# Optimization experiments

Hardware: AMD Instinct MI355X
Metric: run time of the kernel (lower is better)

## Reference

```python
import jax, jax.numpy as jnp
import numpy as np

B, N, C, H, NRES = 32, 1024, 384, 1024, 20
NTAB = 21  # 20 aa + unknown, per AlphaFold residue_constants


def setup_inputs() -> dict:
    key = jax.random.key(0)
    ks = jax.random.split(key, 16)
    s = 0.02
    inp = {}
    inp['act'] = jax.random.normal(ks[0], (B, N, C), jnp.float32)
    inp['angles'] = jax.random.normal(ks[1], (B, N, 7, 2), jnp.float32)
    inp['rigids'] = jax.random.normal(ks[2], (B, N, 7), jnp.float32)
    inp['fixed_mask'] = jax.random.randint(ks[3], (B, N), 0, 2, jnp.int32)
    inp['seq_t'] = jax.random.randint(ks[4], (B, N), 0, NRES, jnp.int32)
    inp['residx_atom37_to_atom14'] = jax.random.randint(ks[5], (B, N, 37), 0, 14, jnp.int32)
    inp['ln_g'] = jnp.ones((C,), jnp.float32)
    inp['ln_b'] = jnp.zeros((C,), jnp.float32)
    inp['w1'] = jax.random.normal(ks[6], (C, H), jnp.float32) * s
    inp['b1'] = jnp.zeros((H,), jnp.float32)
    inp['w2'] = jax.random.normal(ks[7], (H, H), jnp.float32) * s
    inp['b2'] = jnp.zeros((H,), jnp.float32)
    inp['w3'] = jax.random.normal(ks[8], (H, NRES), jnp.float32) * s
    inp['b3'] = jnp.zeros((NRES,), jnp.float32)
    # stand-in residue_constants tables (same shapes/dtypes as AlphaFold's)
    inp['default_frames'] = jax.random.normal(ks[9], (NTAB, 8, 4, 4), jnp.float32)
    inp['group_idx'] = jax.random.randint(ks[10], (NTAB, 14), 0, 8, jnp.int32)
    inp['atom14_mask'] = (jax.random.uniform(ks[11], (NTAB, 14)) > 0.3).astype(jnp.float32)
    inp['atom37_mask'] = (jax.random.uniform(ks[12], (NTAB, 37)) > 0.3).astype(jnp.float32)
    inp['lit_positions'] = jax.random.normal(ks[13], (NTAB, 14, 3), jnp.float32)
    return inp


def quat_to_rot(q):
    q = q / jnp.sqrt(jnp.sum(q * q, axis=-1, keepdims=True) + 1e-8)
    w, x, y, z = q[..., 0], q[..., 1], q[..., 2], q[..., 3]
    r = jnp.stack([
        1 - 2 * (y * y + z * z), 2 * (x * y - w * z), 2 * (x * z + w * y),
        2 * (x * y + w * z), 1 - 2 * (x * x + z * z), 2 * (y * z - w * x),
        2 * (x * z - w * y), 2 * (y * z + w * x), 1 - 2 * (x * x + y * y)
    ], axis=-1)
    return r.reshape(q.shape[:-1] + (3, 3))


def compose(r1, t1, r2, t2):
    # rigid composition: (r1, t1) o (r2, t2)
    return (jnp.einsum('...ij,...jk->...ik', r1, r2),
            jnp.einsum('...ij,...j->...i', r1, t2) + t1)


def reference(act, angles, rigids, fixed_mask, seq_t, residx_atom37_to_atom14,
              ln_g, ln_b, w1, b1, w2, b2, w3, b3,
              default_frames, group_idx, atom14_mask, atom37_mask, lit_positions):
    # --- small MLP head ---
    mu = jnp.mean(act, axis=-1, keepdims=True)
    var = jnp.var(act, axis=-1, keepdims=True)
    h = (act - mu) / jnp.sqrt(var + 1e-5) * ln_g + ln_b
    h = jax.nn.relu(h @ w1 + b1)
    h = jax.nn.relu(h @ w2 + b2)
    logits = h @ w3 + b3                                # [B,N,20]
    p_0t = jax.nn.softmax(logits, axis=-1)
    seq0 = jnp.argmax(p_0t, axis=-1).astype(jnp.int32)
    seq0 = seq0 * (1 - fixed_mask) + seq_t * fixed_mask  # [B,N]

    # --- backbone frame from quaternion rigids ---
    rb = quat_to_rot(rigids[..., :4])                    # [B,N,3,3]
    tb = rigids[..., 4:]                                 # [B,N,3]

    # --- torsion_angles_to_frames ---
    df = default_frames[seq0]                            # [B,N,8,4,4]
    dr, dt = df[..., :3, :3], df[..., :3, 3]
    sin, cos = angles[..., 0], angles[..., 1]            # [B,N,7]
    z1 = jnp.zeros_like(sin[..., :1])
    sin8 = jnp.concatenate([z1, sin], axis=-1)           # backbone group has angle 0
    cos8 = jnp.concatenate([jnp.ones_like(z1), cos], axis=-1)
    zz, oo = jnp.zeros_like(sin8), jnp.ones_like(sin8)
    rx = jnp.stack([oo, zz, zz, zz, cos8, -sin8, zz, sin8, cos8], axis=-1)
    rx = rx.reshape(sin8.shape + (3, 3))                 # rotation about x-axis
    fr = jnp.einsum('bngij,bngjk->bngik', dr, rx)        # frames to backbone (pre-chain)
    ft = dt
    # chain chi2->chi1, chi3->chi2, chi4->chi3
    r5, t5 = compose(fr[..., 4, :, :], ft[..., 4, :], fr[..., 5, :, :], ft[..., 5, :])
    r6, t6 = compose(r5, t5, fr[..., 6, :, :], ft[..., 6, :])
    r7, t7 = compose(r6, t6, fr[..., 7, :, :], ft[..., 7, :])
    frot = jnp.concatenate([fr[..., :5, :, :], r5[..., None, :, :], r6[..., None, :, :], r7[..., None, :, :]], axis=-3)
    ftr = jnp.concatenate([ft[..., :5, :], t5[..., None, :], t6[..., None, :], t7[..., None, :]], axis=-2)
    grot, gtr = compose(rb[..., None, :, :], tb[..., None, :], frot, ftr)  # [B,N,8,3,3],[B,N,8,3]

    # --- frames_and_literature_positions_to_atom14_pos ---
    gi = group_idx[seq0]                                 # [B,N,14]
    ar = jnp.take_along_axis(grot, jnp.broadcast_to(gi[..., None, None], gi.shape + (3, 3)), axis=2)
    at = jnp.take_along_axis(gtr, jnp.broadcast_to(gi[..., None], gi.shape + (3,)), axis=2)
    lit = lit_positions[seq0]                            # [B,N,14,3]
    m14 = atom14_mask[seq0]                              # [B,N,14]
    pred = (jnp.einsum('bnaij,bnaj->bnai', ar, lit) + at) * m14[..., None]

    # --- atom14 -> atom37 gather ---
    idx = residx_atom37_to_atom14
    final = jnp.take_along_axis(pred, jnp.broadcast_to(idx[..., None], idx.shape + (3,)), axis=2)
    m37 = atom37_mask[seq0]                              # [B,N,37]
    return logits, seq0, pred, final, m14, m37
```

## Files before the change

kernel.cpp:

```cpp
#include <hip/hip_runtime.h>
#include <math.h>

#define B_ 32
#define N_ 1024
#define C_ 384
#define H_ 1024
#define NRES 20
#define NTAB 21
#define M_TOTAL (B_*N_)
#define BK 32

typedef __attribute__((ext_vector_type(8))) short bf16x8;
typedef __attribute__((ext_vector_type(4))) float f32x4;

#define GLOAD_LDS(gptr, lptr) \
    __builtin_amdgcn_global_load_lds( \
        (const __attribute__((address_space(1))) void*)(gptr), \
        (__attribute__((address_space(3))) void*)(lptr), 16, 0, 0)

__device__ inline short bf16_rne(float v) {
    unsigned u = __float_as_uint(v);
    unsigned r = u + 0x7fffu + ((u >> 16) & 1u);
    return (short)(r >> 16);
}
__device__ inline void split2(float v, short& h, short& l) {
    unsigned u = __float_as_uint(v);
    unsigned r = (u + 0x7fffu + ((u >> 16) & 1u)) & 0xffff0000u;
    h = (short)(r >> 16);
    l = bf16_rne(v - __uint_as_float(r));
}

__global__ __launch_bounds__(256) void ln_split_kernel(const float* __restrict__ act,
                                                       const float* __restrict__ lng,
                                                       const float* __restrict__ lnb,
                                                       short* __restrict__ Xh,
                                                       short* __restrict__ Xl) {
    int wave = threadIdx.x >> 6;
    int lane = threadIdx.x & 63;
    int row  = blockIdx.x * 4 + wave;
    const float* x = act + (size_t)row * C_;
    float v[6];
    float s = 0.f;
#pragma unroll
    for (int i = 0; i < 6; i++) { v[i] = x[lane + i*64]; s += v[i]; }
#pragma unroll
    for (int off = 32; off > 0; off >>= 1) s += __shfl_xor(s, off, 64);
    float mu = s * (1.0f/384.0f);
    float vs = 0.f;
#pragma unroll
    for (int i = 0; i < 6; i++) { float d = v[i]-mu; vs += d*d; }
#pragma unroll
    for (int off = 32; off > 0; off >>= 1) vs += __shfl_xor(vs, off, 64);
    float rstd = 1.0f / sqrtf(vs * (1.0f/384.0f) + 1e-5f);
#pragma unroll
    for (int i = 0; i < 6; i++) {
        int col = lane + i*64;
        float y = (v[i] - mu) * rstd * lng[col] + lnb[col];
        short h, l; split2(y, h, l);
        Xh[(size_t)row * C_ + col] = h;
        Xl[(size_t)row * C_ + col] = l;
    }
}

__global__ __launch_bounds__(256) void conv_w_kernel(const float* __restrict__ w,
                                                     short* __restrict__ th,
                                                     short* __restrict__ tl,
                                                     int K, int N, int Npad) {
    __shared__ float t[32][33];
    int n0 = blockIdx.x * 32, k0 = blockIdx.y * 32;
    int tx = threadIdx.x & 31, ty = threadIdx.x >> 5;
#pragma unroll
    for (int i = ty; i < 32; i += 8) {
        int k = k0 + i, n = n0 + tx;
        t[i][tx] = (n < N) ? w[(size_t)k * N + n] : 0.f;
    }
    __syncthreads();
#pragma unroll
    for (int i = ty; i < 32; i += 8) {
        int n = n0 + i, k = k0 + tx;
        short h, l; split2(t[tx][i], h, l);
        th[(size_t)n * K + k] = h;
        tl[(size_t)n * K + k] = l;
    }
}

template<bool FUSE>
__global__ __launch_bounds__(512, 2) void presplit_gemm256(
    const short* __restrict__ Ahg, const short* __restrict__ Alg,
    const short* __restrict__ BTh, const short* __restrict__ BTl,
    const float* __restrict__ bias,
    short* __restrict__ Ch, short* __restrict__ Cl,
    int K, int ldc,
    const short* __restrict__ W3h, const short* __restrict__ W3l,
    float* __restrict__ logit_acc, int m0c)
{
    __shared__ short P[4][2][256][32];
    const int BUFS = 256*32;
    int tid = threadIdx.x;
    int m0 = blockIdx.x * 256;
    int n0 = blockIdx.y * 256;
    int lane = tid & 63, wv = tid >> 6;
    int wr = wv >> 2, wc = wv & 3;
    int fm = lane & 15, kg = lane >> 4;

    int pl = wv >> 1, hf = wv & 1;
    const short* gsrc = (pl == 0) ? Ahg : (pl == 1) ? Alg : (pl == 2) ? BTh : BTl;
    int base = (pl < 2) ? m0 : n0;
    int swcb = (lane & 3) ^ ((lane >> 3) & 3);
    const short* gp = gsrc + (size_t)(base + hf*128 + (lane >> 2)) * K + swcb * 8;
    short* lpl = &P[pl][0][0][0] + hf * (128*32);

    int sz = (kg ^ ((fm >> 1) & 3)) * 8;
    const short* raH = &P[0][0][wr*128 + fm][0] + sz;
    const short* raL = &P[1][0][wr*128 + fm][0] + sz;
    const short* rbH = &P[2][0][wc*64  + fm][0] + sz;
    const short* rbL = &P[3][0][wc*64  + fm][0] + sz;

#define STAGE(c, bsel, koff) \
    GLOAD_LDS(gp + (size_t)((c)*16) * K + (koff), lpl + (bsel)*BUFS + (c)*512)

#define TRIPLE(ai, aj, AH, AL, BH, BL) { \
    f32x4 cc = acc[ai][aj]; \
    cc = __builtin_amdgcn_mfma_f32_16x16x32_bf16(AL, BH, cc, 0, 0, 0); \
    cc = __builtin_amdgcn_mfma_f32_16x16x32_bf16(AH, BL, cc, 0, 0, 0); \
    cc = __builtin_amdgcn_mfma_f32_16x16x32_bf16(AH, BH, cc, 0, 0, 0); \
    acc[ai][aj] = cc; }

    f32x4 acc[8][4] = {};
    const int NT = K / BK;

#pragma unroll
    for (int c = 0; c < 8; c++) STAGE(c, 0, 0);

    for (int t = 0; t < NT; ++t) {
        int cur = t & 1, nxt = cur ^ 1;
        size_t koff = (size_t)(t + 1) * BK;
        bool pf = (t + 1 < NT);

        bf16x8 a_h[4], a_l[4], b_h[4], b_l[4];

        if (pf) {
            STAGE(0, nxt, koff); STAGE(1, nxt, koff);
            asm volatile("s_waitcnt vmcnt(2)" ::: "memory");
        } else {
            asm volatile("s_waitcnt vmcnt(0)" ::: "memory");
        }
        __builtin_amdgcn_s_barrier();
        __builtin_amdgcn_sched_barrier(0);
#pragma unroll
        for (int i = 0; i < 4; i++) {
            a_h[i] = *(const bf16x8*)(raH + cur*BUFS + i*512);
            a_l[i] = *(const bf16x8*)(raL + cur*BUFS + i*512);
        }
#pragma unroll
        for (int j = 0; j < 2; j++) {
            b_h[j] = *(const bf16x8*)(rbH + cur*BUFS + j*512);
            b_l[j] = *(const bf16x8*)(rbL + cur*BUFS + j*512);
        }
        __builtin_amdgcn_s_setprio(1);
#pragma unroll
        for (int i = 0; i < 4; i++)
#pragma unroll
            for (int j = 0; j < 2; j++) TRIPLE(i, j, a_h[i], a_l[i], b_h[j], b_l[j]);
        __builtin_amdgcn_s_setprio(0);
        __builtin_amdgcn_s_barrier();

        if (pf) { STAGE(2, nxt, koff); STAGE(3, nxt, koff); }
#pragma unroll
        for (int j = 0; j < 2; j++) {
            b_h[2+j] = *(const bf16x8*)(rbH + cur*BUFS + (2+j)*512);
            b_l[2+j] = *(const bf16x8*)(rbL + cur*BUFS + (2+j)*512);
        }
        __builtin_amdgcn_s_barrier();
        __builtin_amdgcn_s_setprio(1);
#pragma unroll
        for (int i = 0; i < 4; i++)
#pragma unroll
            for (int j = 0; j < 2; j++) TRIPLE(i, 2+j, a_h[i], a_l[i], b_h[2+j], b_l[2+j]);
        __builtin_amdgcn_s_setprio(0);
        __builtin_amdgcn_s_barrier();

        if (pf) { STAGE(4, nxt, koff); STAGE(5, nxt, koff); }
#pragma unroll
        for (int i = 0; i < 4; i++) {
            a_h[i] = *(const bf16x8*)(raH + cur*BUFS + (4+i)*512);
            a_l[i] = *(const bf16x8*)(raL + cur*BUFS + (4+i)*512);
        }
        __builtin_amdgcn_s_barrier();
        __builtin_amdgcn_s_setprio(1);
#pragma unroll
        for (int i = 0; i < 4; i++)
#pragma unroll
            for (int j = 0; j < 2; j++) TRIPLE(4+i, j, a_h[i], a_l[i], b_h[j], b_l[j]);
        __builtin_amdgcn_s_setprio(0);
        __builtin_amdgcn_s_barrier();

        if (pf) { STAGE(6, nxt, koff); STAGE(7, nxt, koff); }
        __builtin_amdgcn_s_barrier();
        __builtin_amdgcn_s_setprio(1);
#pragma unroll
        for (int i = 0; i < 4; i++)
#pragma unroll
            for (int j = 0; j < 2; j++) TRIPLE(4+i, 2+j, a_h[i], a_l[i], b_h[2+j], b_l[2+j]);
        __builtin_amdgcn_s_setprio(0);
        __builtin_amdgcn_s_barrier();
    }

    if (!FUSE) {
#pragma unroll
        for (int i = 0; i < 8; i++)
#pragma unroll
            for (int j = 0; j < 4; j++) {
                int col = n0 + wc*64 + j*16 + fm;
                float bs = bias[col];
#pragma unroll
                for (int r2 = 0; r2 < 4; r2++) {
                    int row = m0 + wr*128 + i*16 + kg*4 + r2;
                    float v = fmaxf(acc[i][j][r2] + bs, 0.f);
                    short h, l; split2(v, h, l);
                    Ch[(size_t)row * ldc + col] = h;
                    Cl[(size_t)row * ldc + col] = l;
                }
            }
    } else {
        unsigned* L32 = (unsigned*)&P[0][0][0][0];
#pragma unroll
        for (int h = 0; h < 2; h++) {
            if (wr == h) {
#pragma unroll
                for (int i = 0; i < 8; i++)
#pragma unroll
                    for (int j = 0; j < 4; j++) {
                        int col = wc*64 + j*16 + fm;
                        float bs = bias[n0 + col];
#pragma unroll
                        for (int r2 = 0; r2 < 4; r2++) {
                            int lr = i*16 + kg*4 + r2;
                            float v = fmaxf(acc[i][j][r2] + bs, 0.f);
                            short sh, sl; split2(v, sh, sl);
                            L32[lr*256 + (col ^ ((lr & 15) << 1))] =
                                ((unsigned)(unsigned short)sh << 16) | (unsigned short)sl;
                        }
                    }
            }
            __syncthreads();
            f32x4 pl0 = {}, pl1 = {};
            int rbase = (wv*16 + fm) * 256;
            int swr = fm << 1;
#pragma unroll
            for (int s = 0; s < 8; s++) {
                int kb = s*32 + kg*8;
                bf16x8 A_h, A_l;
#pragma unroll
                for (int c = 0; c < 8; c++) {
                    unsigned u = L32[rbase + ((kb + c) ^ swr)];
                    A_h[c] = (short)(u >> 16);
                    A_l[c] = (short)(u & 0xffffu);
                }
                size_t wk = (size_t)(n0 + kb);
                bf16x8 B0h = *(const bf16x8*)&W3h[(size_t)fm * H_ + wk];
                bf16x8 B0l = *(const bf16x8*)&W3l[(size_t)fm * H_ + wk];
                bf16x8 B1h = *(const bf16x8*)&W3h[(size_t)(16 + fm) * H_ + wk];
                bf16x8 B1l = *(const bf16x8*)&W3l[(size_t)(16 + fm) * H_ + wk];
                pl0 = __builtin_amdgcn_mfma_f32_16x16x32_bf16(A_l, B0h, pl0, 0, 0, 0);
                pl0 = __builtin_amdgcn_mfma_f32_16x16x32_bf16(A_h, B0l, pl0, 0, 0, 0);
                pl0 = __builtin_amdgcn_mfma_f32_16x16x32_bf16(A_h, B0h, pl0, 0, 0, 0);
                pl1 = __builtin_amdgcn_mfma_f32_16x16x32_bf16(A_l, B1h, pl1, 0, 0, 0);
                pl1 = __builtin_amdgcn_mfma_f32_16x16x32_bf16(A_h, B1l, pl1, 0, 0, 0);
                pl1 = __builtin_amdgcn_mfma_f32_16x16x32_bf16(A_h, B1h, pl1, 0, 0, 0);
            }
            int growb = m0c + m0 + h*128 + wv*16 + kg*4;
#pragma unroll
            for (int r2 = 0; r2 < 4; r2++)
                atomicAdd(&logit_acc[(size_t)(growb + r2) * NRES + fm], pl0[r2]);
            if (fm < 4) {
#pragma unroll
                for (int r2 = 0; r2 < 4; r2++)
                    atomicAdd(&logit_acc[(size_t)(growb + r2) * NRES + 16 + fm], pl1[r2]);
            }
            __syncthreads();
        }
    }
#undef STAGE
#undef TRIPLE
}

__global__ __launch_bounds__(256) void argmax_kernel(
    float* __restrict__ logits, const float* __restrict__ b3,
    const int* __restrict__ fixed_mask, const int* __restrict__ seq_t,
    float* __restrict__ seq_out, int* __restrict__ seq_int, int m0c)
{
    int grow = m0c + blockIdx.x * 256 + threadIdx.x;
    float* lg = logits + (size_t)grow * NRES;
    float best = -1e30f; int bi = 0;
#pragma unroll
    for (int n = 0; n < NRES; n++) {
        float s = lg[n] + b3[n];
        lg[n] = s;
        if (s > best) { best = s; bi = n; }
    }
    int fmk = fixed_mask[grow];
    int sv = fmk ? seq_t[grow] : bi;
    seq_int[grow] = sv;
    seq_out[grow] = (float)sv;
}

__global__ __launch_bounds__(256) void geom_atom_kernel(
    const float* __restrict__ angles, const float* __restrict__ rigids,
    const int* __restrict__ seq0i,
    const float* __restrict__ dframes, const int* __restrict__ gidx,
    const float* __restrict__ a14m, const float* __restrict__ litp,
    float* __restrict__ out_pred, float* __restrict__ out_m14)
{
    __shared__ float sdf[NTAB*8*16];
    __shared__ int   sgi[NTAB*14];
    __shared__ float sm14[NTAB*14];
    __shared__ float slit[NTAB*14*3];
    for (int i = threadIdx.x; i < NTAB*128; i += 256) sdf[i] = dframes[i];
    for (int i = threadIdx.x; i < NTAB*14; i += 256) { sgi[i] = gidx[i]; sm14[i] = a14m[i]; }
    for (int i = threadIdx.x; i < NTAB*42; i += 256) slit[i] = litp[i];
    __syncthreads();

    int idx = blockIdx.x * 256 + threadIdx.x;
    int p = idx / 14, a = idx - p * 14;
    int s = seq0i[p];

    const float* rg = rigids + (size_t)p * 7;
    float qw = rg[0], qx = rg[1], qy = rg[2], qz = rg[3];
    float tbx = rg[4], tby = rg[5], tbz = rg[6];
    float qn = 1.0f / sqrtf(qw*qw + qx*qx + qy*qy + qz*qz + 1e-8f);
    qw *= qn; qx *= qn; qy *= qn; qz *= qn;
    float rb[9];
    rb[0] = 1.f - 2.f*(qy*qy + qz*qz); rb[1] = 2.f*(qx*qy - qw*qz); rb[2] = 2.f*(qx*qz + qw*qy);
    rb[3] = 2.f*(qx*qy + qw*qz); rb[4] = 1.f - 2.f*(qx*qx + qz*qz); rb[5] = 2.f*(qy*qz - qw*qx);
    rb[6] = 2.f*(qx*qz - qw*qy); rb[7] = 2.f*(qy*qz + qw*qx); rb[8] = 1.f - 2.f*(qx*qx + qy*qy);

    const float* ang = angles + (size_t)p * 14;
    int g = sgi[s*14 + a];

    auto build = [&](int gg, float* r, float* t) {
        const float* df = &sdf[(s*8 + gg)*16];
        float c, sn;
        if (gg == 0) { c = 1.f; sn = 0.f; }
        else { sn = ang[(gg-1)*2 + 0]; c = ang[(gg-1)*2 + 1]; }
#pragma unroll
        for (int i = 0; i < 3; i++) {
            float d0 = df[i*4+0], d1 = df[i*4+1], d2 = df[i*4+2];
            r[i*3+0] = d0;
            r[i*3+1] = d1*c + d2*sn;
            r[i*3+2] = d2*c - d1*sn;
            t[i] = df[i*4+3];
        }
    };

    float R[9], T[3];
    if (g < 5) {
        build(g, R, T);
    } else {
        build(4, R, T);
        for (int gg = 5; gg <= g; gg++) {
            float f[9], tt[3], r2[9], t2[3];
            build(gg, f, tt);
#pragma unroll
            for (int i = 0; i < 3; i++) {
#pragma unroll
                for (int j = 0; j < 3; j++)
                    r2[i*3+j] = R[i*3+0]*f[0*3+j] + R[i*3+1]*f[1*3+j] + R[i*3+2]*f[2*3+j];
                t2[i] = R[i*3+0]*tt[0] + R[i*3+1]*tt[1] + R[i*3+2]*tt[2] + T[i];
            }
#pragma unroll
            for (int i = 0; i < 9; i++) R[i] = r2[i];
#pragma unroll
            for (int i = 0; i < 3; i++) T[i] = t2[i];
        }
    }

    float Rg[9], Tg[3];
#pragma unroll
    for (int i = 0; i < 3; i++) {
#pragma unroll
        for (int j = 0; j < 3; j++)
            Rg[i*3+j] = rb[i*3+0]*R[0*3+j] + rb[i*3+1]*R[1*3+j] + rb[i*3+2]*R[2*3+j];
        Tg[i] = rb[i*3+0]*T[0] + rb[i*3+1]*T[1] + rb[i*3+2]*T[2];
    }
    Tg[0] += tbx; Tg[1] += tby; Tg[2] += tbz;

    float m  = sm14[s*14 + a];
    float lx = slit[(s*14 + a)*3 + 0];
    float ly = slit[(s*14 + a)*3 + 1];
    float lz = slit[(s*14 + a)*3 + 2];
    out_pred[(size_t)idx*3 + 0] = (Rg[0]*lx + Rg[1]*ly + Rg[2]*lz + Tg[0]) * m;
    out_pred[(size_t)idx*3 + 1] = (Rg[3]*lx + Rg[4]*ly + Rg[5]*lz + Tg[1]) * m;
    out_pred[(size_t)idx*3 + 2] = (Rg[6]*lx + Rg[7]*ly + Rg[8]*lz + Tg[2]) * m;
    out_m14[idx] = m;
}

__global__ __launch_bounds__(256) void final_gather_kernel(
    const int* __restrict__ seq0i, const int* __restrict__ residx,
    const float* __restrict__ a37m, const float* __restrict__ out_pred,
    float* __restrict__ out_final, float* __restrict__ out_m37)
{
    __shared__ float sm37[NTAB*37];
    for (int i = threadIdx.x; i < NTAB*37; i += 256) sm37[i] = a37m[i];
    __syncthreads();

    int idx = blockIdx.x * 256 + threadIdx.x;
    int p = idx / 37, a = idx - p * 37;
    int s = seq0i[p];
    int id = residx[idx];
    const float* src = out_pred + ((size_t)p*14 + id)*3;
    out_final[(size_t)idx*3 + 0] = src[0];
    out_final[(size_t)idx*3 + 1] = src[1];
    out_final[(size_t)idx*3 + 2] = src[2];
    out_m37[idx] = sm37[s*37 + a];
}

extern "C" void kernel_launch(void* const* d_in, const int* in_sizes, int n_in,
                              void* d_out, int out_size, void* d_ws, size_t ws_size,
                              hipStream_t stream) {
    const float* act        = (const float*)d_in[0];
    const float* angles     = (const float*)d_in[1];
    const float* rigids     = (const float*)d_in[2];
    const int*   fixed_mask = (const int*)d_in[3];
    const int*   seq_t      = (const int*)d_in[4];
    const int*   residx     = (const int*)d_in[5];
    const float* lng        = (const float*)d_in[6];
    const float* lnb        = (const float*)d_in[7];
    const float* w1         = (const float*)d_in[8];
    const float* b1         = (const float*)d_in[9];
    const float* w2         = (const float*)d_in[10];
    const float* b2         = (const float*)d_in[11];
    const float* w3         = (const float*)d_in[12];
    const float* b3         = (const float*)d_in[13];
    const float* dfr        = (const float*)d_in[14];
    const int*   gidx       = (const int*)d_in[15];
    const float* a14m       = (const float*)d_in[16];
    const float* a37m       = (const float*)d_in[17];
    const float* litp       = (const float*)d_in[18];

    float* out        = (float*)d_out;
    float* out_logits = out;
    float* out_seq    = out_logits + (size_t)M_TOTAL * NRES;
    float* out_pred   = out_seq    + (size_t)M_TOTAL;
    float* out_final  = out_pred   + (size_t)M_TOTAL * 42;
    float* out_m14    = out_final  + (size_t)M_TOTAL * 111;
    float* out_m37    = out_m14    + (size_t)M_TOTAL * 14;

    char* wsp = (char*)d_ws;
    int*   seq0i = (int*)wsp;   wsp += (size_t)M_TOTAL * sizeof(int);
    short* w1h   = (short*)wsp; wsp += (size_t)H_ * C_ * sizeof(short);
    short* w1l   = (short*)wsp; wsp += (size_t)H_ * C_ * sizeof(short);
    short* w2h   = (short*)wsp; wsp += (size_t)H_ * H_ * sizeof(short);
    short* w2l   = (short*)wsp; wsp += (size_t)H_ * H_ * sizeof(short);
    short* w3h   = (short*)wsp; wsp += (size_t)128 * H_ * sizeof(short);
    short* w3l   = (short*)wsp; wsp += (size_t)128 * H_ * sizeof(short);
    short* Xh    = (short*)wsp; wsp += (size_t)M_TOTAL * C_ * sizeof(short);
    short* Xl    = (short*)wsp; wsp += (size_t)M_TOTAL * C_ * sizeof(short);

    size_t fixed_bytes = (size_t)(wsp - (char*)d_ws);
    size_t per_row = 2ull * H_ * sizeof(short);
    size_t avail = ws_size - fixed_bytes;
    int chunkM = 4096;
    if (avail >= (size_t)M_TOTAL * per_row)      chunkM = M_TOTAL;
    else if (avail >= 16384ull * per_row)        chunkM = 16384;
    else if (avail >= 8192ull * per_row)         chunkM = 8192;

    short* H1h = (short*)wsp; wsp += (size_t)chunkM * H_ * sizeof(short);
    short* H1l = (short*)wsp;

    hipMemsetAsync(out_logits, 0, (size_t)M_TOTAL * NRES * sizeof(float), stream);

    conv_w_kernel<<<dim3(H_/32, C_/32), 256, 0, stream>>>(w1, w1h, w1l, C_, H_, H_);
    conv_w_kernel<<<dim3(H_/32, H_/32), 256, 0, stream>>>(w2, w2h, w2l, H_, H_, H_);
    conv_w_kernel<<<dim3(128/32, H_/32), 256, 0, stream>>>(w3, w3h, w3l, H_, NRES, 128);

    ln_split_kernel<<<M_TOTAL/4, 256, 0, stream>>>(act, lng, lnb, Xh, Xl);

    for (int c = 0; c < M_TOTAL / chunkM; c++) {
        int m0 = c * chunkM;
        presplit_gemm256<false><<<dim3(chunkM/256, H_/256), 512, 0, stream>>>(
            Xh + (size_t)m0 * C_, Xl + (size_t)m0 * C_, w1h, w1l, b1,
            H1h, H1l, C_, H_, nullptr, nullptr, nullptr, 0);
        presplit_gemm256<true><<<dim3(chunkM/256, H_/256), 512, 0, stream>>>(
            H1h, H1l, w2h, w2l, b2,
            nullptr, nullptr, H_, 0, w3h, w3l, out_logits, m0);
        argmax_kernel<<<chunkM/256, 256, 0, stream>>>(
            out_logits, b3, fixed_mask, seq_t, out_seq, seq0i, m0);
    }

    geom_atom_kernel<<<(M_TOTAL*14)/256, 256, 0, stream>>>(
        angles, rigids, seq0i, dfr, gidx, a14m, litp, out_pred, out_m14);
    final_gather_kernel<<<(M_TOTAL*37)/256, 256, 0, stream>>>(
        seq0i, residx, a37m, out_pred, out_final, out_m37);
}
```

Before: 460.1 us.

## Fuse prep and tail kernels, replace logit atomics with per-tile partial buffer

Merges the three weight-conversion launches and the layernorm split into one prep kernel. The fused GEMM now writes per-N-tile partial logits to a buffer instead of issuing atomicAdds, which also drops the memset. A single tail kernel sums the partials, applies the bias and argmax, then runs the geometry and the atom37 gather from shared memory. This removes several launches, the atomics and the round trip of pred through global memory. In exchange it needs an extra partial buffer, which may alias Xh when the whole batch fits in one chunk, and the tail does its argmax with only 16 threads per block.

```diff
diff --git a/kernel.cpp b/kernel.cpp
--- a/kernel.cpp
+++ b/kernel.cpp
@@ -30,44 +30,10 @@
     l = bf16_rne(v - __uint_as_float(r));
 }
 
-__global__ __launch_bounds__(256) void ln_split_kernel(const float* __restrict__ act,
-                                                       const float* __restrict__ lng,
-                                                       const float* __restrict__ lnb,
-                                                       short* __restrict__ Xh,
-                                                       short* __restrict__ Xl) {
-    int wave = threadIdx.x >> 6;
-    int lane = threadIdx.x & 63;
-    int row  = blockIdx.x * 4 + wave;
-    const float* x = act + (size_t)row * C_;
-    float v[6];
-    float s = 0.f;
-#pragma unroll
-    for (int i = 0; i < 6; i++) { v[i] = x[lane + i*64]; s += v[i]; }
-#pragma unroll
-    for (int off = 32; off > 0; off >>= 1) s += __shfl_xor(s, off, 64);
-    float mu = s * (1.0f/384.0f);
-    float vs = 0.f;
-#pragma unroll
-    for (int i = 0; i < 6; i++) { float d = v[i]-mu; vs += d*d; }
-#pragma unroll
-    for (int off = 32; off > 0; off >>= 1) vs += __shfl_xor(vs, off, 64);
-    float rstd = 1.0f / sqrtf(vs * (1.0f/384.0f) + 1e-5f);
-#pragma unroll
-    for (int i = 0; i < 6; i++) {
-        int col = lane + i*64;
-        float y = (v[i] - mu) * rstd * lng[col] + lnb[col];
-        short h, l; split2(y, h, l);
-        Xh[(size_t)row * C_ + col] = h;
-        Xl[(size_t)row * C_ + col] = l;
-    }
-}
-
-__global__ __launch_bounds__(256) void conv_w_kernel(const float* __restrict__ w,
-                                                     short* __restrict__ th,
-                                                     short* __restrict__ tl,
-                                                     int K, int N, int Npad) {
-    __shared__ float t[32][33];
-    int n0 = blockIdx.x * 32, k0 = blockIdx.y * 32;
+__device__ inline void conv_body(const float* __restrict__ w,
+                                 short* __restrict__ th, short* __restrict__ tl,
+                                 int K, int N, int n0, int k0,
+                                 float (*t)[33]) {
     int tx = threadIdx.x & 31, ty = threadIdx.x >> 5;
 #pragma unroll
     for (int i = ty; i < 32; i += 8) {
@@ -81,6 +47,55 @@
         short h, l; split2(t[tx][i], h, l);
         th[(size_t)n * K + k] = h;
         tl[(size_t)n * K + k] = l;
+    }
+}
+
+__global__ __launch_bounds__(256) void prep_kernel(
+    const float* __restrict__ w1, const float* __restrict__ w2,
+    const float* __restrict__ w3,
+    short* __restrict__ w1h, short* __restrict__ w1l,
+    short* __restrict__ w2h, short* __restrict__ w2l,
+    short* __restrict__ w3h, short* __restrict__ w3l,
+    const float* __restrict__ act, const float* __restrict__ lng,
+    const float* __restrict__ lnb,
+    short* __restrict__ Xh, short* __restrict__ Xl)
+{
+    __shared__ float t[32][33];
+    int bid = blockIdx.x;
+    if (bid < 384) {
+        conv_body(w1, w1h, w1l, C_, H_, (bid & 31) * 32, (bid >> 5) * 32, t);
+    } else if (bid < 1408) {
+        int b = bid - 384;
+        conv_body(w2, w2h, w2l, H_, H_, (b & 31) * 32, (b >> 5) * 32, t);
+    } else if (bid < 1536) {
+        int b = bid - 1408;
+        conv_body(w3, w3h, w3l, H_, NRES, (b & 3) * 32, (b >> 2) * 32, t);
+    } else {
+        int wave = threadIdx.x >> 6;
+        int lane = threadIdx.x & 63;
+        int row  = (bid - 1536) * 4 + wave;
+        const float* x = act + (size_t)row * C_;
+        float v[6];
+        float s = 0.f;
+#pragma unroll
+        for (int i = 0; i < 6; i++) { v[i] = x[lane + i*64]; s += v[i]; }
+#pragma unroll
+        for (int off = 32; off > 0; off >>= 1) s += __shfl_xor(s, off, 64);
+        float mu = s * (1.0f/384.0f);
+        float vs = 0.f;
+#pragma unroll
+        for (int i = 0; i < 6; i++) { float d = v[i]-mu; vs += d*d; }
+#pragma unroll
+        for (int off = 32; off > 0; off >>= 1) vs += __shfl_xor(vs, off, 64);
+        float rstd = 1.0f / sqrtf(vs * (1.0f/384.0f) + 1e-5f);
+#pragma unroll
+        for (int i = 0; i < 6; i++) {
+            int col = lane + i*64;
+            float y = (v[i] - mu) * rstd * lng[col] + lnb[col];
+            short h, l; split2(y, h, l);
+            Xh[(size_t)row * C_ + col] = h;
+            Xl[(size_t)row * C_ + col] = l;
+        }
     }
 }
 
@@ -92,7 +107,7 @@
     short* __restrict__ Ch, short* __restrict__ Cl,
     int K, int ldc,
     const short* __restrict__ W3h, const short* __restrict__ W3l,
-    float* __restrict__ logit_acc, int m0c)
+    float* __restrict__ pbuf, int m0c)
 {
     __shared__ short P[4][2][256][32];
     const int BUFS = 256*32;
@@ -270,13 +285,14 @@
                 pl1 = __builtin_amdgcn_mfma_f32_16x16x32_bf16(A_h, B1h, pl1, 0, 0, 0);
             }
             int growb = m0c + m0 + h*128 + wv*16 + kg*4;
+            float* pp = pbuf + ((size_t)blockIdx.y * M_TOTAL + growb) * 32;
 #pragma unroll
             for (int r2 = 0; r2 < 4; r2++)
-                atomicAdd(&logit_acc[(size_t)(growb + r2) * NRES + fm], pl0[r2]);
+                pp[(size_t)r2 * 32 + fm] = pl0[r2];
             if (fm < 4) {
 #pragma unroll
                 for (int r2 = 0; r2 < 4; r2++)
-                    atomicAdd(&logit_acc[(size_t)(growb + r2) * NRES + 16 + fm], pl1[r2]);
+                    pp[(size_t)r2 * 32 + 16 + fm] = pl1[r2];
             }
             __syncthreads();
         }
@@ -285,134 +301,144 @@
 #undef TRIPLE
 }
 
-__global__ __launch_bounds__(256) void argmax_kernel(
-    float* __restrict__ logits, const float* __restrict__ b3,
+__global__ __launch_bounds__(256) void tail_kernel(
+    const float* __restrict__ Pbuf, const float* __restrict__ b3,
     const int* __restrict__ fixed_mask, const int* __restrict__ seq_t,
-    float* __restrict__ seq_out, int* __restrict__ seq_int, int m0c)
-{
-    int grow = m0c + blockIdx.x * 256 + threadIdx.x;
-    float* lg = logits + (size_t)grow * NRES;
-    float best = -1e30f; int bi = 0;
-#pragma unroll
-    for (int n = 0; n < NRES; n++) {
-        float s = lg[n] + b3[n];
-        lg[n] = s;
-        if (s > best) { best = s; bi = n; }
-    }
-    int fmk = fixed_mask[grow];
-    int sv = fmk ? seq_t[grow] : bi;
-    seq_int[grow] = sv;
-    seq_out[grow] = (float)sv;
-}
-
-__global__ __launch_bounds__(256) void geom_atom_kernel(
     const float* __restrict__ angles, const float* __restrict__ rigids,
-    const int* __restrict__ seq0i,
-    const float* __restrict__ dframes, const int* __restrict__ gidx,
-    const float* __restrict__ a14m, const float* __restrict__ litp,
-    float* __restrict__ out_pred, float* __restrict__ out_m14)
+    const int* __restrict__ residx, const float* __restrict__ dframes,
+    const int* __restrict__ gidx, const float* __restrict__ a14m,
+    const float* __restrict__ a37m, const float* __restrict__ litp,
+    float* __restrict__ out_logits, float* __restrict__ out_seq,
+    float* __restrict__ out_pred, float* __restrict__ out_final,
+    float* __restrict__ out_m14, float* __restrict__ out_m37)
 {
     __shared__ float sdf[NTAB*8*16];
     __shared__ int   sgi[NTAB*14];
     __shared__ float sm14[NTAB*14];
+    __shared__ float sm37[NTAB*37];
     __shared__ float slit[NTAB*14*3];
+    __shared__ float spred[16][14][3];
+    __shared__ int   sseq[16];
+
     for (int i = threadIdx.x; i < NTAB*128; i += 256) sdf[i] = dframes[i];
     for (int i = threadIdx.x; i < NTAB*14; i += 256) { sgi[i] = gidx[i]; sm14[i] = a14m[i]; }
+    for (int i = threadIdx.x; i < NTAB*37; i += 256) sm37[i] = a37m[i];
     for (int i = threadIdx.x; i < NTAB*42; i += 256) slit[i] = litp[i];
     __syncthreads();
 
-    int idx = blockIdx.x * 256 + threadIdx.x;
-    int p = idx / 14, a = idx - p * 14;
-    int s = seq0i[p];
-
-    const float* rg = rigids + (size_t)p * 7;
-    float qw = rg[0], qx = rg[1], qy = rg[2], qz = rg[3];
-    float tbx = rg[4], tby = rg[5], tbz = rg[6];
-    float qn = 1.0f / sqrtf(qw*qw + qx*qx + qy*qy + qz*qz + 1e-8f);
-    qw *= qn; qx *= qn; qy *= qn; qz *= qn;
-    float rb[9];
-    rb[0] = 1.f - 2.f*(qy*qy + qz*qz); rb[1] = 2.f*(qx*qy - qw*qz); rb[2] = 2.f*(qx*qz + qw*qy);
-    rb[3] = 2.f*(qx*qy + qw*qz); rb[4] = 1.f - 2.f*(qx*qx + qz*qz); rb[5] = 2.f*(qy*qz - qw*qx);
-    rb[6] = 2.f*(qx*qz - qw*qy); rb[7] = 2.f*(qy*qz + qw*qx); rb[8] = 1.f - 2.f*(qx*qx + qy*qy);
-
-    const float* ang = angles + (size_t)p * 14;
-    int g = sgi[s*14 + a];
-
-    auto build = [&](int gg, float* r, float* t) {
-        const float* df = &sdf[(s*8 + gg)*16];
-        float c, sn;
-        if (gg == 0) { c = 1.f; sn = 0.f; }
-        else { sn = ang[(gg-1)*2 + 0]; c = ang[(gg-1)*2 + 1]; }
+    int pbase = blockIdx.x * 16;
+
+    if (threadIdx.x < 16) {
+        int p = pbase + threadIdx.x;
+        float best = -1e30f; int bi = 0;
+        float* lg = out_logits + (size_t)p * NRES;
+#pragma unroll
+        for (int n = 0; n < NRES; n++) {
+            float s = b3[n];
+#pragma unroll
+            for (int k = 0; k < 4; k++)
+                s += Pbuf[((size_t)k * M_TOTAL + p) * 32 + n];
+            lg[n] = s;
+            if (s > best) { best = s; bi = n; }
+        }
+        int sv = fixed_mask[p] ? seq_t[p] : bi;
+        sseq[threadIdx.x] = sv;
+        out_seq[p] = (float)sv;
+    }
+    __syncthreads();
+
+    if (threadIdx.x < 224) {
+        int pt = threadIdx.x / 14, a = threadIdx.x % 14;
+        int p = pbase + pt;
+        int s = sseq[pt];
+        int idx = p * 14 + a;
+
+        const float* rg = rigids + (size_t)p * 7;
+        float qw = rg[0], qx = rg[1], qy = rg[2], qz = rg[3];
+        float tbx = rg[4], tby = rg[5], tbz = rg[6];
+        float qn = 1.0f / sqrtf(qw*qw + qx*qx + qy*qy + qz*qz + 1e-8f);
+        qw *= qn; qx *= qn; qy *= qn; qz *= qn;
+        float rb[9];
+        rb[0] = 1.f - 2.f*(qy*qy + qz*qz); rb[1] = 2.f*(qx*qy - qw*qz); rb[2] = 2.f*(qx*qz + qw*qy);
+        rb[3] = 2.f*(qx*qy + qw*qz); rb[4] = 1.f - 2.f*(qx*qx + qz*qz); rb[5] = 2.f*(qy*qz - qw*qx);
+        rb[6] = 2.f*(qx*qz - qw*qy); rb[7] = 2.f*(qy*qz + qw*qx); rb[8] = 1.f - 2.f*(qx*qx + qy*qy);
+
+        const float* ang = angles + (size_t)p * 14;
+        int g = sgi[s*14 + a];
+
+        auto build = [&](int gg, float* r, float* t) {
+            const float* df = &sdf[(s*8 + gg)*16];
+            float c, sn;
+            if (gg == 0) { c = 1.f; sn = 0.f; }
+            else { sn = ang[(gg-1)*2 + 0]; c = ang[(gg-1)*2 + 1]; }
+#pragma unroll
+            for (int i = 0; i < 3; i++) {
+                float d0 = df[i*4+0], d1 = df[i*4+1], d2 = df[i*4+2];
+                r[i*3+0] = d0;
+                r[i*3+1] = d1*c + d2*sn;
+                r[i*3+2] = d2*c - d1*sn;
+                t[i] = df[i*4+3];
+            }
+        };
+
+        float R[9], T[3];
+        if (g < 5) {
+            build(g, R, T);
+        } else {
+            build(4, R, T);
+            for (int gg = 5; gg <= g; gg++) {
+                float f[9], tt[3], r2[9], t2[3];
+                build(gg, f, tt);
+#pragma unroll
+                for (int i = 0; i < 3; i++) {
+#pragma unroll
+                    for (int j = 0; j < 3; j++)
+                        r2[i*3+j] = R[i*3+0]*f[0*3+j] + R[i*3+1]*f[1*3+j] + R[i*3+2]*f[2*3+j];
+                    t2[i] = R[i*3+0]*tt[0] + R[i*3+1]*tt[1] + R[i*3+2]*tt[2] + T[i];
+                }
+#pragma unroll
+                for (int i = 0; i < 9; i++) R[i] = r2[i];
+#pragma unroll
+                for (int i = 0; i < 3; i++) T[i] = t2[i];
+            }
+        }
+
+        float Rg[9], Tg[3];
 #pragma unroll
         for (int i = 0; i < 3; i++) {
-            float d0 = df[i*4+0], d1 = df[i*4+1], d2 = df[i*4+2];
-            r[i*3+0] = d0;
-            r[i*3+1] = d1*c + d2*sn;
-            r[i*3+2] = d2*c - d1*sn;
-            t[i] = df[i*4+3];
-        }
-    };
-
-    float R[9], T[3];
-    if (g < 5) {
-        build(g, R, T);
-    } else {
-        build(4, R, T);
-        for (int gg = 5; gg <= g; gg++) {
-            float f[9], tt[3], r2[9], t2[3];
-            build(gg, f, tt);
-#pragma unroll
-            for (int i = 0; i < 3; i++) {
-#pragma unroll
-                for (int j = 0; j < 3; j++)
-                    r2[i*3+j] = R[i*3+0]*f[0*3+j] + R[i*3+1]*f[1*3+j] + R[i*3+2]*f[2*3+j];
-                t2[i] = R[i*3+0]*tt[0] + R[i*3+1]*tt[1] + R[i*3+2]*tt[2] + T[i];
-            }
-#pragma unroll
-            for (int i = 0; i < 9; i++) R[i] = r2[i];
-#pragma unroll
-            for (int i = 0; i < 3; i++) T[i] = t2[i];
-        }
-    }
-
-    float Rg[9], Tg[3];
-#pragma unroll
-    for (int i = 0; i < 3; i++) {
-#pragma unroll
-        for (int j = 0; j < 3; j++)
-            Rg[i*3+j] = rb[i*3+0]*R[0*3+j] + rb[i*3+1]*R[1*3+j] + rb[i*3+2]*R[2*3+j];
-        Tg[i] = rb[i*3+0]*T[0] + rb[i*3+1]*T[1] + rb[i*3+2]*T[2];
-    }
-    Tg[0] += tbx; Tg[1] += tby; Tg[2] += tbz;
-
-    float m  = sm14[s*14 + a];
-    float lx = slit[(s*14 + a)*3 + 0];
-    float ly = slit[(s*14 + a)*3 + 1];
-    float lz = slit[(s*14 + a)*3 + 2];
-    out_pred[(size_t)idx*3 + 0] = (Rg[0]*lx + Rg[1]*ly + Rg[2]*lz + Tg[0]) * m;
-    out_pred[(size_t)idx*3 + 1] = (Rg[3]*lx + Rg[4]*ly + Rg[5]*lz + Tg[1]) * m;
-    out_pred[(size_t)idx*3 + 2] = (Rg[6]*lx + Rg[7]*ly + Rg[8]*lz + Tg[2]) * m;
-    out_m14[idx] = m;
-}
-
-__global__ __launch_bounds__(256) void final_gather_kernel(
-    const int* __restrict__ seq0i, const int* __restrict__ residx,
-    const float* __restrict__ a37m, const float* __restrict__ out_pred,
-    float* __restrict__ out_final, float* __restrict__ out_m37)
-{
-    __shared__ float sm37[NTAB*37];
-    for (int i = threadIdx.x; i < NTAB*37; i += 256) sm37[i] = a37m[i];
+#pragma unroll
+            for (int j = 0; j < 3; j++)
+                Rg[i*3+j] = rb[i*3+0]*R[0*3+j] + rb[i*3+1]*R[1*3+j] + rb[i*3+2]*R[2*3+j];
+            Tg[i] = rb[i*3+0]*T[0] + rb[i*3+1]*T[1] + rb[i*3+2]*T[2];
+        }
+        Tg[0] += tbx; Tg[1] += tby; Tg[2] += tbz;
+
+        float m  = sm14[s*14 + a];
+        float lx = slit[(s*14 + a)*3 + 0];
+        float ly = slit[(s*14 + a)*3 + 1];
+        float lz = slit[(s*14 + a)*3 + 2];
+        float px = (Rg[0]*lx + Rg[1]*ly + Rg[2]*lz + Tg[0]) * m;
+        float py = (Rg[3]*lx + Rg[4]*ly + Rg[5]*lz + Tg[1]) * m;
+        float pz = (Rg[6]*lx + Rg[7]*ly + Rg[8]*lz + Tg[2]) * m;
+        out_pred[(size_t)idx*3 + 0] = px;
+        out_pred[(size_t)idx*3 + 1] = py;
+        out_pred[(size_t)idx*3 + 2] = pz;
+        spred[pt][a][0] = px; spred[pt][a][1] = py; spred[pt][a][2] = pz;
+        out_m14[idx] = m;
+    }
     __syncthreads();
 
-    int idx = blockIdx.x * 256 + threadIdx.x;
-    int p = idx / 37, a = idx - p * 37;
-    int s = seq0i[p];
-    int id = residx[idx];
-    const float* src = out_pred + ((size_t)p*14 + id)*3;
-    out_final[(size_t)idx*3 + 0] = src[0];
-    out_final[(size_t)idx*3 + 1] = src[1];
-    out_final[(size_t)idx*3 + 2] = src[2];
-    out_m37[idx] = sm37[s*37 + a];
+    for (int i = threadIdx.x; i < 16*37; i += 256) {
+        int pt = i / 37, a = i - pt * 37;
+        int p = pbase + pt;
+        int s = sseq[pt];
+        int idx = p * 37 + a;
+        int id = residx[idx];
+        out_final[(size_t)idx*3 + 0] = spred[pt][id][0];
+        out_final[(size_t)idx*3 + 1] = spred[pt][id][1];
+        out_final[(size_t)idx*3 + 2] = spred[pt][id][2];
+        out_m37[idx] = sm37[s*37 + a];
+    }
 }
 
 extern "C" void kernel_launch(void* const* d_in, const int* in_sizes, int n_in,
@@ -447,7 +473,6 @@
     float* out_m37    = out_m14    + (size_t)M_TOTAL * 14;
 
     char* wsp = (char*)d_ws;
-    int*   seq0i = (int*)wsp;   wsp += (size_t)M_TOTAL * sizeof(int);
     short* w1h   = (short*)wsp; wsp += (size_t)H_ * C_ * sizeof(short);
     short* w1l   = (short*)wsp; wsp += (size_t)H_ * C_ * sizeof(short);
     short* w2h   = (short*)wsp; wsp += (size_t)H_ * H_ * sizeof(short);
@@ -459,22 +484,20 @@
 
     size_t fixed_bytes = (size_t)(wsp - (char*)d_ws);
     size_t per_row = 2ull * H_ * sizeof(short);
+    size_t PB = 4ull * M_TOTAL * 32 * sizeof(float);
     size_t avail = ws_size - fixed_bytes;
-    int chunkM = 4096;
-    if (avail >= (size_t)M_TOTAL * per_row)      chunkM = M_TOTAL;
-    else if (avail >= 16384ull * per_row)        chunkM = 16384;
-    else if (avail >= 8192ull * per_row)         chunkM = 8192;
+    int chunkM;
+    if (avail >= (size_t)M_TOTAL * per_row)           chunkM = M_TOTAL;
+    else if (avail >= 16384ull * per_row + PB)        chunkM = 16384;
+    else if (avail >= 8192ull * per_row + PB)         chunkM = 8192;
+    else                                              chunkM = 4096;
 
     short* H1h = (short*)wsp; wsp += (size_t)chunkM * H_ * sizeof(short);
-    short* H1l = (short*)wsp;
-
-    hipMemsetAsync(out_logits, 0, (size_t)M_TOTAL * NRES * sizeof(float), stream);
-
-    conv_w_kernel<<<dim3(H_/32, C_/32), 256, 0, stream>>>(w1, w1h, w1l, C_, H_, H_);
-    conv_w_kernel<<<dim3(H_/32, H_/32), 256, 0, stream>>>(w2, w2h, w2l, H_, H_, H_);
-    conv_w_kernel<<<dim3(128/32, H_/32), 256, 0, stream>>>(w3, w3h, w3l, H_, NRES, 128);
-
-    ln_split_kernel<<<M_TOTAL/4, 256, 0, stream>>>(act, lng, lnb, Xh, Xl);
+    short* H1l = (short*)wsp; wsp += (size_t)chunkM * H_ * sizeof(short);
+    float* Pbuf = (chunkM == M_TOTAL) ? (float*)Xh : (float*)wsp;
+
+    prep_kernel<<<1536 + M_TOTAL/4, 256, 0, stream>>>(
+        w1, w2, w3, w1h, w1l, w2h, w2l, w3h, w3l, act, lng, lnb, Xh, Xl);
 
     for (int c = 0; c < M_TOTAL / chunkM; c++) {
         int m0 = c * chunkM;
@@ -483,13 +506,11 @@
             H1h, H1l, C_, H_, nullptr, nullptr, nullptr, 0);
         presplit_gemm256<true><<<dim3(chunkM/256, H_/256), 512, 0, stream>>>(
             H1h, H1l, w2h, w2l, b2,
-            nullptr, nullptr, H_, 0, w3h, w3l, out_logits, m0);
-        argmax_kernel<<<chunkM/256, 256, 0, stream>>>(
-            out_logits, b3, fixed_mask, seq_t, out_seq, seq0i, m0);
-    }
-
-    geom_atom_kernel<<<(M_TOTAL*14)/256, 256, 0, stream>>>(
-        angles, rigids, seq0i, dfr, gidx, a14m, litp, out_pred, out_m14);
-    final_gather_kernel<<<(M_TOTAL*37)/256, 256, 0, stream>>>(
-        seq0i, residx, a37m, out_pred, out_final, out_m37);
-}
+            nullptr, nullptr, H_, 0, w3h, w3l, Pbuf, m0);
+    }
+
+    tail_kernel<<<M_TOTAL/16, 256, 0, stream>>>(
+        Pbuf, b3, fixed_mask, seq_t, angles, rigids, residx,
+        dfr, gidx, a14m, a37m, litp,
+        out_logits, out_seq, out_pred, out_final, out_m14, out_m37);
+}
```

Measured after the change: 446.5 us. 2.9% less time.
